# Kernel optimization log

Measured on AMD Instinct MI355X. Metric: run time of the kernel, lower is better.

Reference implementation:

```python
import jax, jax.numpy as jnp
import numpy as np

N = 50000      # nodes
K = 8          # ensemble slices
DIN = 128
DOUT = 128
E = 800000     # edges (avg degree 16)


def setup_inputs() -> dict:
    key = jax.random.key(0)
    k0, k1, k2 = jax.random.split(key, 3)
    inputs = jax.random.normal(k0, (N, K, DIN), dtype=jnp.float32)
    edge_index = jax.random.randint(k1, (2, E), 0, N, dtype=jnp.int32)
    W = jax.random.normal(k2, (DIN, DOUT), dtype=jnp.float32) / np.sqrt(DIN).astype(np.float32)
    b = jnp.zeros((DOUT,), dtype=jnp.float32)
    return {"inputs": inputs, "edge_index": edge_index, "W": W, "b": b}


def reference(inputs, edge_index, W, b):
    # GraphConvolutionK forward: for each of K slices, GCNConv(x, edge_index) then ReLU.
    # GCNConv (PyG default): add self-loops, D^{-1/2} A D^{-1/2} (x W) + b.
    n_nodes = inputs.shape[0]
    loops = jnp.arange(n_nodes, dtype=edge_index.dtype)
    src = jnp.concatenate([edge_index[0], loops])   # [E+N]
    dst = jnp.concatenate([edge_index[1], loops])   # [E+N]

    deg = jax.ops.segment_sum(jnp.ones_like(dst, dtype=jnp.float32), dst,
                              num_segments=n_nodes)            # in-degree incl. self-loop
    dinv = jnp.where(deg > 0, jax.lax.rsqrt(deg), 0.0)         # deg^{-1/2}
    norm = dinv[src] * dinv[dst]                               # [E+N] per-edge coefficient

    x_k = jnp.transpose(inputs, (1, 0, 2))  # [K, N, Din] — scan over K to bound memory

    def step(_, x):                          # x: [N, Din]
        h = x @ W                            # feature transform [N, Dout]
        msg = h[src] * norm[:, None]         # gather + scale   [E+N, Dout]
        agg = jax.ops.segment_sum(msg, dst, num_segments=n_nodes) + b
        return None, jax.nn.relu(agg)

    _, outs = jax.lax.scan(step, None, x_k)  # [K, N, Dout]
    return jnp.transpose(outs, (1, 0, 2))    # [N, K, Dout]
```

## Files before the change

### kernel.cpp

```cpp
#include <hip/hip_runtime.h>

#define KSL 8
#define DIN 128
#define DOUT 128

typedef __attribute__((ext_vector_type(8))) short bf16x8;
typedef __attribute__((ext_vector_type(4))) float f32x4;

static __device__ __forceinline__ unsigned int f2b_bits(float f) {
    unsigned int u = __float_as_uint(f);
    return (u + 0x7fffu + ((u >> 16) & 1u)) >> 16;
}

static __device__ __forceinline__ float amax8(float4 a0, float4 a1,
                                              float4 b0, float4 b1) {
    float m = fmaxf(fmaxf(fmaxf(fabsf(a0.x), fabsf(a0.y)), fmaxf(fabsf(a0.z), fabsf(a0.w))),
                    fmaxf(fmaxf(fabsf(a1.x), fabsf(a1.y)), fmaxf(fabsf(a1.z), fabsf(a1.w))));
    m = fmaxf(m, fmaxf(fmaxf(fmaxf(fabsf(b0.x), fabsf(b0.y)), fmaxf(fabsf(b0.z), fabsf(b0.w))),
                       fmaxf(fmaxf(fabsf(b1.x), fabsf(b1.y)), fmaxf(fabsf(b1.z), fabsf(b1.w)))));
    return m;
}

static __device__ __forceinline__ unsigned int pack4(float4 v, float inv) {
    int q0 = __float2int_rn(v.x * inv) + 128, q1 = __float2int_rn(v.y * inv) + 128;
    int q2 = __float2int_rn(v.z * inv) + 128, q3 = __float2int_rn(v.w * inv) + 128;
    return (q0 & 0xff) | ((q1 & 0xff) << 8) | ((q2 & 0xff) << 16) |
           ((unsigned)(q3 & 0xff) << 24);
}

__global__ __launch_bounds__(256) void quant_deg(
        const float* __restrict__ x, char* __restrict__ xq,
        float* __restrict__ scales, int N,
        const int* __restrict__ dst, int E, int* __restrict__ deg) {
    long long tid = (long long)blockIdx.x * blockDim.x + threadIdx.x;
    int e4 = E >> 2;
    if (tid < e4) {
        int4 d = ((const int4*)dst)[tid];
        atomicAdd(&deg[d.x], 1);
        atomicAdd(&deg[d.y], 1);
        atomicAdd(&deg[d.z], 1);
        atomicAdd(&deg[d.w], 1);
    }
    if (tid < (E & 3)) atomicAdd(&deg[dst[e4 * 4 + tid]], 1);

    int w = (int)(tid >> 6);
    int lane = (int)(tid & 63);
    if (w >= N) return;

    int ks = lane >> 3, chunk = lane & 7;
    int g = chunk >> 1, ktb = (chunk & 1) * 2;
    const float* p0 = x + (size_t)w * (KSL * DIN) + (size_t)ks * DIN + ktb * 32 + g * 8;
    float4 a0 = ((const float4*)p0)[0];
    float4 a1 = ((const float4*)p0)[1];
    float4 b0 = ((const float4*)(p0 + 32))[0];
    float4 b1 = ((const float4*)(p0 + 32))[1];
    float m = amax8(a0, a1, b0, b1);
    #pragma unroll
    for (int s = 32; s > 0; s >>= 1) m = fmaxf(m, __shfl_xor(m, s));

    float inv = (m > 0.f) ? 127.f / m : 0.f;
    uint4 o;
    o.x = pack4(a0, inv);
    o.y = pack4(a1, inv);
    o.z = pack4(b0, inv);
    o.w = pack4(b1, inv);
    *(uint4*)(xq + (size_t)w * 1024 + lane * 16) = o;
    if (lane == 0) scales[w] = m * (1.f / 127.f);
}

__global__ __launch_bounds__(256) void partial_sums(
        const int* __restrict__ deg, int N, int CHK,
        const float* __restrict__ scales,
        float* __restrict__ dinv, float* __restrict__ sd,
        int* __restrict__ blockSums) {
    __shared__ int red[256];
    int b = blockIdx.x, t = threadIdx.x;
    int start = b * CHK;
    int end = min(start + CHK, N);
    int s = 0;
    for (int i = start + t; i < end; i += 256) {
        int d = deg[i];
        float di = rsqrtf((float)(d + 1));
        dinv[i] = di;
        sd[i] = di * scales[i];
        s += d;
    }
    red[t] = s;
    __syncthreads();
    #pragma unroll
    for (int st = 128; st > 0; st >>= 1) {
        if (t < st) red[t] += red[t + st];
        __syncthreads();
    }
    if (t == 0) blockSums[b] = red[0];
}

__global__ __launch_bounds__(256) void scan_bases(
        int* __restrict__ blockSums, int nb, int* __restrict__ off, int N) {
    __shared__ int buf[256];
    int t = threadIdx.x;
    int v = (t < nb) ? blockSums[t] : 0;
    buf[t] = v;
    __syncthreads();
    #pragma unroll
    for (int st = 1; st < 256; st <<= 1) {
        int u = (t >= st) ? buf[t - st] : 0;
        __syncthreads();
        buf[t] += u;
        __syncthreads();
    }
    if (t < nb) blockSums[t] = buf[t] - v;
    if (t == 255) off[N] = buf[255];
}

__global__ __launch_bounds__(256) void write_off(
        const int* __restrict__ deg, int N, int CHK,
        const int* __restrict__ blockSums, int* __restrict__ off) {
    __shared__ int buf[256];
    int b = blockIdx.x, t = threadIdx.x;
    int start = b * CHK;
    int end = min(start + CHK, N);
    int run = blockSums[b];
    for (int base = start; base < end; base += 256) {
        int i = base + t;
        int d = (i < end) ? deg[i] : 0;
        __syncthreads();
        buf[t] = d;
        __syncthreads();
        #pragma unroll
        for (int st = 1; st < 256; st <<= 1) {
            int u = (t >= st) ? buf[t - st] : 0;
            __syncthreads();
            buf[t] += u;
            __syncthreads();
        }
        if (i < end) off[i] = run + buf[t] - d;
        run += buf[255];
    }
}

static __device__ __forceinline__ void fill_edge(
        int s, int d, const float* __restrict__ dinv,
        const float* __restrict__ sd, const int* __restrict__ off,
        int* __restrict__ cursor, int2* __restrict__ csr) {
    int pos = atomicAdd(&cursor[d], 1);
    csr[off[d] + pos] = make_int2(s, __float_as_int(sd[s] * dinv[d]));
}

__global__ __launch_bounds__(256) void fill_csr(
        const int* __restrict__ src, const int* __restrict__ dst, int E,
        const int* __restrict__ off, int* __restrict__ cursor,
        const float* __restrict__ dinv, const float* __restrict__ sd,
        int2* __restrict__ csr) {
    int i = blockIdx.x * blockDim.x + threadIdx.x;
    int e4 = E >> 2;
    if (i < e4) {
        int4 s4 = ((const int4*)src)[i];
        int4 d4 = ((const int4*)dst)[i];
        fill_edge(s4.x, d4.x, dinv, sd, off, cursor, csr);
        fill_edge(s4.y, d4.y, dinv, sd, off, cursor, csr);
        fill_edge(s4.z, d4.z, dinv, sd, off, cursor, csr);
        fill_edge(s4.w, d4.w, dinv, sd, off, cursor, csr);
    }
    if (i < (E & 3)) {
        int e = e4 * 4 + i;
        fill_edge(src[e], dst[e], dinv, sd, off, cursor, csr);
    }
}

__global__ __launch_bounds__(256) void aggemm(
        const char* __restrict__ xq, const float* __restrict__ scales,
        const int* __restrict__ off, const int2* __restrict__ csr,
        const float* __restrict__ dinv,
        const float* __restrict__ W, const float* __restrict__ bias,
        int N, float* __restrict__ out) {
    __shared__ unsigned short Wt[128 * 128];

    int t = threadIdx.x;
    {
        int c = t & 127;
        int khalf = t >> 7;
        #pragma unroll
        for (int kc = 0; kc < 8; kc++) {
            int k0 = khalf * 64 + kc * 8;
            unsigned int u0 = f2b_bits(W[(size_t)(k0 + 0) * 128 + c]) |
                             (f2b_bits(W[(size_t)(k0 + 1) * 128 + c]) << 16);
            unsigned int u1 = f2b_bits(W[(size_t)(k0 + 2) * 128 + c]) |
                             (f2b_bits(W[(size_t)(k0 + 3) * 128 + c]) << 16);
            unsigned int u2 = f2b_bits(W[(size_t)(k0 + 4) * 128 + c]) |
                             (f2b_bits(W[(size_t)(k0 + 5) * 128 + c]) << 16);
            unsigned int u3 = f2b_bits(W[(size_t)(k0 + 6) * 128 + c]) |
                             (f2b_bits(W[(size_t)(k0 + 7) * 128 + c]) << 16);
            int byte = c * 256 + k0 * 2;
            byte ^= (c & 7) << 4;
            *(uint4*)((char*)Wt + byte) = make_uint4(u0, u1, u2, u3);
        }
    }
    __syncthreads();

    int wid = t >> 6, lane = t & 63;
    int pair = blockIdx.x * 4 + wid;
    int n0 = pair * 2;
    if (n0 >= N) return;

    int rit = lane & 15;
    int g   = lane >> 4;
    int mynode = n0 + (rit >> 3);
    if (mynode >= N) mynode = n0;
    int kslice = rit & 7;

    int offAu = __builtin_amdgcn_readfirstlane(off[n0]);
    int offMu = __builtin_amdgcn_readfirstlane(off[n0 + 1]);
    int offEu = __builtin_amdgcn_readfirstlane((n0 + 2 <= N) ? off[n0 + 2] : 0);
    int degAu = offMu - offAu;
    int degBu = (n0 + 1 < N) ? (offEu - offMu) : 0;
    int maxd  = max(degAu, degBu);
    int mydeg = (rit < 8) ? degAu : degBu;
    bool isA  = (rit < 8);
    const int2* csrA = csr + offAu;
    const int2* csrB = csr + offMu;

    const size_t rofs = (size_t)kslice * 128 + g * 32;

    float acc[32];
    float wsum;

    #define UB0(w) ((float)((w) & 0xffu))
    #define UB1(w) ((float)(((w) >> 8) & 0xffu))
    #define UB2(w) ((float)(((w) >> 16) & 0xffu))
    #define UB3(w) ((float)((w) >> 24))

    {
        float ds = dinv[mynode];
        float selfw = ds * ds * scales[mynode];
        wsum = selfw;
        const uint4* rb = (const uint4*)(xq + (size_t)mynode * 1024 + rofs);
        uint4 q0 = rb[0];
        uint4 q1 = rb[1];
        #define UNPK0(wrd, base)                                             \
            acc[(base) + 0] = UB0(wrd) * selfw;                              \
            acc[(base) + 1] = UB1(wrd) * selfw;                              \
            acc[(base) + 2] = UB2(wrd) * selfw;                              \
            acc[(base) + 3] = UB3(wrd) * selfw;
        UNPK0(q0.x, 0)  UNPK0(q0.y, 4)  UNPK0(q0.z, 8)  UNPK0(q0.w, 12)
        UNPK0(q1.x, 16) UNPK0(q1.y, 20) UNPK0(q1.z, 24) UNPK0(q1.w, 28)
        #undef UNPK0
    }

    #define UNPK(wrd, base, wg)                                              \
        acc[(base) + 0] += UB0(wrd) * (wg);                                  \
        acc[(base) + 1] += UB1(wrd) * (wg);                                  \
        acc[(base) + 2] += UB2(wrd) * (wg);                                  \
        acc[(base) + 3] += UB3(wrd) * (wg);

    int j = 0;
    for (; j + 1 < maxd; j += 2) {
        int2 eA0 = csrA[j];
        int2 eA1 = csrA[j + 1];
        int2 eB0 = csrB[j];
        int2 eB1 = csrB[j + 1];

        bool v0 = (j < mydeg);
        bool v1 = (j + 1 < mydeg);
        int   s0 = isA ? eA0.x : eB0.x;
        float w0 = __int_as_float(isA ? eA0.y : eB0.y);
        int   s1 = isA ? eA1.x : eB1.x;
        float w1 = __int_as_float(isA ? eA1.y : eB1.y);
        s0 = v0 ? s0 : mynode;  w0 = v0 ? w0 : 0.f;
        s1 = v1 ? s1 : mynode;  w1 = v1 ? w1 : 0.f;
        wsum += w0;
        wsum += w1;

        const uint4* rb0 = (const uint4*)(xq + (size_t)s0 * 1024 + rofs);
        const uint4* rb1 = (const uint4*)(xq + (size_t)s1 * 1024 + rofs);
        uint4 q00 = rb0[0];
        uint4 q01 = rb0[1];
        uint4 q10 = rb1[0];
        uint4 q11 = rb1[1];

        UNPK(q00.x, 0, w0)  UNPK(q00.y, 4, w0)  UNPK(q00.z, 8, w0)  UNPK(q00.w, 12, w0)
        UNPK(q01.x, 16, w0) UNPK(q01.y, 20, w0) UNPK(q01.z, 24, w0) UNPK(q01.w, 28, w0)
        UNPK(q10.x, 0, w1)  UNPK(q10.y, 4, w1)  UNPK(q10.z, 8, w1)  UNPK(q10.w, 12, w1)
        UNPK(q11.x, 16, w1) UNPK(q11.y, 20, w1) UNPK(q11.z, 24, w1) UNPK(q11.w, 28, w1)
    }
    if (j < maxd) {
        int2 eA = csrA[j];
        int2 eB = csrB[j];
        bool v0 = (j < mydeg);
        int   s0 = isA ? eA.x : eB.x;
        float w0 = __int_as_float(isA ? eA.y : eB.y);
        s0 = v0 ? s0 : mynode;  w0 = v0 ? w0 : 0.f;
        wsum += w0;
        const uint4* rb0 = (const uint4*)(xq + (size_t)s0 * 1024 + rofs);
        uint4 q00 = rb0[0];
        uint4 q01 = rb0[1];
        UNPK(q00.x, 0, w0)  UNPK(q00.y, 4, w0)  UNPK(q00.z, 8, w0)  UNPK(q00.w, 12, w0)
        UNPK(q01.x, 16, w0) UNPK(q01.y, 20, w0) UNPK(q01.z, 24, w0) UNPK(q01.w, 28, w0)
    }
    #undef UNPK
    #undef UB0
    #undef UB1
    #undef UB2
    #undef UB3

    {
        float corr = 128.f * wsum;
        #pragma unroll
        for (int i = 0; i < 32; i++) acc[i] -= corr;
    }

    bf16x8 afrag[4];
    #pragma unroll
    for (int kt = 0; kt < 4; kt++) {
        #pragma unroll
        for (int e = 0; e < 8; e++)
            afrag[kt][e] = (short)f2b_bits(acc[kt * 8 + e]);
    }

    long long r0 = (long long)n0 * 8;
    #pragma unroll
    for (int ct = 0; ct < 8; ct++) {
        int c = ct * 16 + rit;
        f32x4 acct = {0.f, 0.f, 0.f, 0.f};
        #pragma unroll
        for (int kt = 0; kt < 4; kt++) {
            int byte = c * 256 + kt * 64 + g * 16;
            byte ^= (c & 7) << 4;
            bf16x8 bfrag = *(const bf16x8*)((const char*)Wt + byte);
            acct = __builtin_amdgcn_mfma_f32_16x16x32_bf16(afrag[kt], bfrag, acct, 0, 0, 0);
        }
        float bv = bias[c];
        #pragma unroll
        for (int r = 0; r < 4; r++) {
            long long row = r0 + g * 4 + r;
            out[row * 128 + c] = fmaxf(acct[r] + bv, 0.f);
        }
    }
}

extern "C" void kernel_launch(void* const* d_in, const int* in_sizes, int n_in,
                              void* d_out, int out_size, void* d_ws, size_t ws_size,
                              hipStream_t stream) {
    const float* x  = (const float*)d_in[0];
    const int*   ei = (const int*)d_in[1];
    const float* W  = (const float*)d_in[2];
    const float* b  = (const float*)d_in[3];
    float* out = (float*)d_out;

    int N = in_sizes[0] / (KSL * DIN);
    int E = in_sizes[1] / 2;
    const int* src = ei;
    const int* dst = ei + E;

    char* ws = (char*)d_ws;
    size_t o = 0;
    auto alloc = [&](size_t bytes) -> void* {
        o = (o + 255) & ~(size_t)255;
        void* p = ws + o;
        o += bytes;
        return p;
    };
    int*   deg       = (int*)alloc((size_t)N * 4);
    int*   cursor    = (int*)alloc((size_t)N * 4);
    int*   off       = (int*)alloc((size_t)(N + 1) * 4);
    float* dinv      = (float*)alloc((size_t)N * 4);
    float* scales    = (float*)alloc((size_t)N * 4);
    float* sd        = (float*)alloc((size_t)N * 4);
    int*   blockSums = (int*)alloc((size_t)256 * 4);
    int2*  csr       = (int2*)alloc((size_t)(E + 1) * 8);
    char*  xq        = (char*)alloc((size_t)N * KSL * DIN);

    size_t z_bytes = (size_t)((char*)cursor - (char*)deg) + (size_t)N * 4;
    hipMemsetAsync(deg, 0, z_bytes, stream);

    long long qthreads = (long long)N * 64;
    int qblocks = (int)((qthreads + 255) / 256);
    quant_deg<<<qblocks, 256, 0, stream>>>(x, xq, scales, N, dst, E, deg);

    int CHK = (N + 255) / 256;
    partial_sums<<<256, 256, 0, stream>>>(deg, N, CHK, scales, dinv, sd, blockSums);
    scan_bases<<<1, 256, 0, stream>>>(blockSums, 256, off, N);
    write_off<<<256, 256, 0, stream>>>(deg, N, CHK, blockSums, off);
    fill_csr<<<((E >> 2) + 255) / 256, 256, 0, stream>>>(src, dst, E, off, cursor,
                                                         dinv, sd, csr);

    int pairs = (N + 1) / 2;
    int blocks = (pairs + 3) / 4;
    aggemm<<<blocks, 256, 0, stream>>>(xq, scales, off, csr, dinv, W, b, N, out);
}
```

Measured before the change: 297.2 us.

## Pair nodes by degree via histogram permutation and coalesce quantization loads

Builds a degree histogram and a counting-sort permutation so each wavefront processes two nodes of similar in-degree. This aims to cut divergence from the max-degree loop when paired nodes have very different degrees. The quantization kernel now reads input rows with fully coalesced float4 loads and scatters the packed bytes into the same layout as before. Costs are extra atomics, a second scan, and output writes that are no longer contiguous across wavefronts.

Measured after the change: 428.9 us. 44.3% more time.

```diff
diff --git a/kernel.cpp b/kernel.cpp
--- a/kernel.cpp
+++ b/kernel.cpp
@@ -12,13 +12,8 @@
     return (u + 0x7fffu + ((u >> 16) & 1u)) >> 16;
 }
 
-static __device__ __forceinline__ float amax8(float4 a0, float4 a1,
-                                              float4 b0, float4 b1) {
-    float m = fmaxf(fmaxf(fmaxf(fabsf(a0.x), fabsf(a0.y)), fmaxf(fabsf(a0.z), fabsf(a0.w))),
-                    fmaxf(fmaxf(fabsf(a1.x), fabsf(a1.y)), fmaxf(fabsf(a1.z), fabsf(a1.w))));
-    m = fmaxf(m, fmaxf(fmaxf(fmaxf(fabsf(b0.x), fabsf(b0.y)), fmaxf(fabsf(b0.z), fabsf(b0.w))),
-                       fmaxf(fmaxf(fabsf(b1.x), fabsf(b1.y)), fmaxf(fabsf(b1.z), fabsf(b1.w)))));
-    return m;
+static __device__ __forceinline__ float amax4(float4 v) {
+    return fmaxf(fmaxf(fabsf(v.x), fabsf(v.y)), fmaxf(fabsf(v.z), fabsf(v.w)));
 }
 
 static __device__ __forceinline__ unsigned int pack4(float4 v, float inv) {
@@ -47,24 +42,26 @@
     int lane = (int)(tid & 63);
     if (w >= N) return;
 
-    int ks = lane >> 3, chunk = lane & 7;
-    int g = chunk >> 1, ktb = (chunk & 1) * 2;
-    const float* p0 = x + (size_t)w * (KSL * DIN) + (size_t)ks * DIN + ktb * 32 + g * 8;
-    float4 a0 = ((const float4*)p0)[0];
-    float4 a1 = ((const float4*)p0)[1];
-    float4 b0 = ((const float4*)(p0 + 32))[0];
-    float4 b1 = ((const float4*)(p0 + 32))[1];
-    float m = amax8(a0, a1, b0, b1);
+    const float4* xr = (const float4*)(x + (size_t)w * (KSL * DIN));
+    float4 f0 = xr[lane];
+    float4 f1 = xr[64 + lane];
+    float4 f2 = xr[128 + lane];
+    float4 f3 = xr[192 + lane];
+
+    float m = fmaxf(fmaxf(amax4(f0), amax4(f1)), fmaxf(amax4(f2), amax4(f3)));
     #pragma unroll
     for (int s = 32; s > 0; s >>= 1) m = fmaxf(m, __shfl_xor(m, s));
 
     float inv = (m > 0.f) ? 127.f / m : 0.f;
-    uint4 o;
-    o.x = pack4(a0, inv);
-    o.y = pack4(a1, inv);
-    o.z = pack4(b0, inv);
-    o.w = pack4(b1, inv);
-    *(uint4*)(xq + (size_t)w * 1024 + lane * 16) = o;
+
+    int l5 = lane & 31;
+    int hi = lane >> 5;
+    int base = ((l5 >> 1) & 3) * 32 + (l5 >> 3) * 8 + (l5 & 1) * 4;
+    char* orow = xq + (size_t)w * 1024;
+    *(unsigned int*)(orow + (0 + hi) * 128 + base) = pack4(f0, inv);
+    *(unsigned int*)(orow + (2 + hi) * 128 + base) = pack4(f1, inv);
+    *(unsigned int*)(orow + (4 + hi) * 128 + base) = pack4(f2, inv);
+    *(unsigned int*)(orow + (6 + hi) * 128 + base) = pack4(f3, inv);
     if (lane == 0) scales[w] = m * (1.f / 127.f);
 }
 
@@ -72,9 +69,12 @@
         const int* __restrict__ deg, int N, int CHK,
         const float* __restrict__ scales,
         float* __restrict__ dinv, float* __restrict__ sd,
-        int* __restrict__ blockSums) {
+        int* __restrict__ blockSums, int* __restrict__ hist) {
     __shared__ int red[256];
+    __shared__ int lhist[256];
     int b = blockIdx.x, t = threadIdx.x;
+    lhist[t] = 0;
+    __syncthreads();
     int start = b * CHK;
     int end = min(start + CHK, N);
     int s = 0;
@@ -84,9 +84,11 @@
         dinv[i] = di;
         sd[i] = di * scales[i];
         s += d;
+        atomicAdd(&lhist[min(d, 255)], 1);
     }
     red[t] = s;
     __syncthreads();
+    if (lhist[t] > 0) atomicAdd(&hist[t], lhist[t]);
     #pragma unroll
     for (int st = 128; st > 0; st >>= 1) {
         if (t < st) red[t] += red[t + st];
@@ -96,7 +98,8 @@
 }
 
 __global__ __launch_bounds__(256) void scan_bases(
-        int* __restrict__ blockSums, int nb, int* __restrict__ off, int N) {
+        int* __restrict__ blockSums, int nb, int* __restrict__ off, int N,
+        const int* __restrict__ hist, int* __restrict__ histBase) {
     __shared__ int buf[256];
     int t = threadIdx.x;
     int v = (t < nb) ? blockSums[t] : 0;
@@ -111,11 +114,25 @@
     }
     if (t < nb) blockSums[t] = buf[t] - v;
     if (t == 255) off[N] = buf[255];
+    __syncthreads();
+    int h = hist[t];
+    buf[t] = h;
+    __syncthreads();
+    #pragma unroll
+    for (int st = 1; st < 256; st <<= 1) {
+        int u = (t >= st) ? buf[t - st] : 0;
+        __syncthreads();
+        buf[t] += u;
+        __syncthreads();
+    }
+    histBase[t] = buf[t] - h;
 }
 
 __global__ __launch_bounds__(256) void write_off(
         const int* __restrict__ deg, int N, int CHK,
-        const int* __restrict__ blockSums, int* __restrict__ off) {
+        const int* __restrict__ blockSums, int* __restrict__ off,
+        const int* __restrict__ histBase, int* __restrict__ histCursor,
+        int* __restrict__ perm) {
     __shared__ int buf[256];
     int b = blockIdx.x, t = threadIdx.x;
     int start = b * CHK;
@@ -134,7 +151,12 @@
             buf[t] += u;
             __syncthreads();
         }
-        if (i < end) off[i] = run + buf[t] - d;
+        if (i < end) {
+            off[i] = run + buf[t] - d;
+            int dd = min(d, 255);
+            int rank = histBase[dd] + atomicAdd(&histCursor[dd], 1);
+            perm[rank] = i;
+        }
         run += buf[255];
     }
 }
@@ -171,7 +193,7 @@
 __global__ __launch_bounds__(256) void aggemm(
         const char* __restrict__ xq, const float* __restrict__ scales,
         const int* __restrict__ off, const int2* __restrict__ csr,
-        const float* __restrict__ dinv,
+        const float* __restrict__ dinv, const int* __restrict__ perm,
         const float* __restrict__ W, const float* __restrict__ bias,
         int N, float* __restrict__ out) {
     __shared__ unsigned short Wt[128 * 128];
@@ -200,25 +222,29 @@
 
     int wid = t >> 6, lane = t & 63;
     int pair = blockIdx.x * 4 + wid;
-    int n0 = pair * 2;
-    if (n0 >= N) return;
+    int ia = pair * 2;
+    if (ia >= N) return;
+    int ib = min(ia + 1, N - 1);
+
+    int na = __builtin_amdgcn_readfirstlane(perm[ia]);
+    int nb = __builtin_amdgcn_readfirstlane(perm[ib]);
 
     int rit = lane & 15;
     int g   = lane >> 4;
-    int mynode = n0 + (rit >> 3);
-    if (mynode >= N) mynode = n0;
+    bool isA = (rit < 8);
+    int mynode = isA ? na : nb;
     int kslice = rit & 7;
 
-    int offAu = __builtin_amdgcn_readfirstlane(off[n0]);
-    int offMu = __builtin_amdgcn_readfirstlane(off[n0 + 1]);
-    int offEu = __builtin_amdgcn_readfirstlane((n0 + 2 <= N) ? off[n0 + 2] : 0);
-    int degAu = offMu - offAu;
-    int degBu = (n0 + 1 < N) ? (offEu - offMu) : 0;
+    int offA0 = __builtin_amdgcn_readfirstlane(off[na]);
+    int offA1 = __builtin_amdgcn_readfirstlane(off[na + 1]);
+    int offB0 = __builtin_amdgcn_readfirstlane(off[nb]);
+    int offB1 = __builtin_amdgcn_readfirstlane(off[nb + 1]);
+    int degAu = offA1 - offA0;
+    int degBu = offB1 - offB0;
     int maxd  = max(degAu, degBu);
-    int mydeg = (rit < 8) ? degAu : degBu;
-    bool isA  = (rit < 8);
-    const int2* csrA = csr + offAu;
-    const int2* csrB = csr + offMu;
+    int mydeg = isA ? degAu : degBu;
+    const int2* csrA = csr + offA0;
+    const int2* csrB = csr + offB0;
 
     const size_t rofs = (size_t)kslice * 128 + g * 32;
 
@@ -317,7 +343,7 @@
             afrag[kt][e] = (short)f2b_bits(acc[kt * 8 + e]);
     }
 
-    long long r0 = (long long)n0 * 8;
+    long long rowbase = (long long)((g >= 2) ? nb : na) * 8 + (g & 1) * 4;
     #pragma unroll
     for (int ct = 0; ct < 8; ct++) {
         int c = ct * 16 + rit;
@@ -332,7 +358,7 @@
         float bv = bias[c];
         #pragma unroll
         for (int r = 0; r < 4; r++) {
-            long long row = r0 + g * 4 + r;
+            long long row = rowbase + r;
             out[row * 128 + c] = fmaxf(acct[r] + bv, 0.f);
         }
     }
@@ -360,17 +386,21 @@
         o += bytes;
         return p;
     };
-    int*   deg       = (int*)alloc((size_t)N * 4);
-    int*   cursor    = (int*)alloc((size_t)N * 4);
-    int*   off       = (int*)alloc((size_t)(N + 1) * 4);
-    float* dinv      = (float*)alloc((size_t)N * 4);
-    float* scales    = (float*)alloc((size_t)N * 4);
-    float* sd        = (float*)alloc((size_t)N * 4);
-    int*   blockSums = (int*)alloc((size_t)256 * 4);
-    int2*  csr       = (int2*)alloc((size_t)(E + 1) * 8);
-    char*  xq        = (char*)alloc((size_t)N * KSL * DIN);
-
-    size_t z_bytes = (size_t)((char*)cursor - (char*)deg) + (size_t)N * 4;
+    int*   deg        = (int*)alloc((size_t)N * 4);
+    int*   cursor     = (int*)alloc((size_t)N * 4);
+    int*   hist       = (int*)alloc((size_t)256 * 4);
+    int*   histCursor = (int*)alloc((size_t)256 * 4);
+    int*   off        = (int*)alloc((size_t)(N + 1) * 4);
+    float* dinv       = (float*)alloc((size_t)N * 4);
+    float* scales     = (float*)alloc((size_t)N * 4);
+    float* sd         = (float*)alloc((size_t)N * 4);
+    int*   blockSums  = (int*)alloc((size_t)256 * 4);
+    int*   histBase   = (int*)alloc((size_t)256 * 4);
+    int*   perm       = (int*)alloc((size_t)N * 4);
+    int2*  csr        = (int2*)alloc((size_t)(E + 1) * 8);
+    char*  xq         = (char*)alloc((size_t)N * KSL * DIN);
+
+    size_t z_bytes = (size_t)((char*)histCursor - (char*)deg) + (size_t)256 * 4;
     hipMemsetAsync(deg, 0, z_bytes, stream);
 
     long long qthreads = (long long)N * 64;
@@ -378,13 +408,16 @@
     quant_deg<<<qblocks, 256, 0, stream>>>(x, xq, scales, N, dst, E, deg);
 
     int CHK = (N + 255) / 256;
-    partial_sums<<<256, 256, 0, stream>>>(deg, N, CHK, scales, dinv, sd, blockSums);
-    scan_bases<<<1, 256, 0, stream>>>(blockSums, 256, off, N);
-    write_off<<<256, 256, 0, stream>>>(deg, N, CHK, blockSums, off);
+    partial_sums<<<256, 256, 0, stream>>>(deg, N, CHK, scales, dinv, sd,
+                                          blockSums, hist);
+    scan_bases<<<1, 256, 0, stream>>>(blockSums, 256, off, N, hist, histBase);
+    write_off<<<256, 256, 0, stream>>>(deg, N, CHK, blockSums, off,
+                                       histBase, histCursor, perm);
     fill_csr<<<((E >> 2) + 255) / 256, 256, 0, stream>>>(src, dst, E, off, cursor,
                                                          dinv, sd, csr);
 
     int pairs = (N + 1) / 2;
     int blocks = (pairs + 3) / 4;
-    aggemm<<<blocks, 256, 0, stream>>>(xq, scales, off, csr, dinv, W, b, N, out);
-}
+    aggemm<<<blocks, 256, 0, stream>>>(xq, scales, off, csr, dinv, perm,
+                                       W, b, N, out);
+}
```
